# Kernel tuning notes

Measured on AMD Instinct MI355X. Metric: run time of the kernel, lower is better.

Reference implementation:

```python
import jax, jax.numpy as jnp
import numpy as np

DIM = 256          # channels
HEADS = 8
KS = 3             # kernel_size
DIL = (1, 2, 3, 4) # dilation rates
ND = len(DIL)
HEAD_DIM = DIM // HEADS
SCALE = HEAD_DIM ** -0.5
DPG = DIM // ND    # channels per dilation group
EPS = 1e-5


def setup_inputs() -> dict:
    key = jax.random.key(0)
    ks = jax.random.split(key, 4)
    B, H, W = 8, 64, 64
    vi = jax.random.normal(ks[0], (B, DIM, H, W), jnp.float32)
    ir = jax.random.normal(ks[1], (B, DIM, H, W), jnp.float32)
    w_qkv = jax.random.normal(ks[2], (3 * DIM, DIM), jnp.float32) * 0.02  # 1x1 conv, no bias (qkv_bias=False)
    proj_w = jax.random.normal(ks[3], (DIM, DIM), jnp.float32) * 0.02     # nn.Linear weight
    proj_b = jnp.zeros((DIM,), jnp.float32)
    ln_g = jnp.ones((DIM,), jnp.float32)
    ln_b = jnp.zeros((DIM,), jnp.float32)
    return dict(vi=vi, ir=ir, w_qkv=w_qkv, proj_w=proj_w, proj_b=proj_b, ln_g=ln_g, ln_b=ln_b)


def _unfold(t, dil):
    # t: [B, d, H, W] -> [B, d, KS*KS, H, W], same layout as nn.Unfold(KS, dil, pad=dil*(KS-1)//2)
    B, d, H, W = t.shape
    pad = dil * (KS - 1) // 2
    tp = jnp.pad(t, ((0, 0), (0, 0), (pad, pad), (pad, pad)))
    patches = [tp[:, :, i * dil:i * dil + H, j * dil:j * dil + W]
               for i in range(KS) for j in range(KS)]
    return jnp.stack(patches, axis=2)


def _dilate_attention(q, k, v, dil):
    # q,k,v: [B, d, H, W] with d = DPG; returns [B, H, W, d]
    B, d, H, W = q.shape
    h = d // HEAD_DIM
    N = H * W
    kk = KS * KS
    qf = q.reshape(B, h, HEAD_DIM, N)                      # b h d n
    kf = _unfold(k, dil).reshape(B, h, HEAD_DIM, kk, N)    # b h d k n
    vf = _unfold(v, dil).reshape(B, h, HEAD_DIM, kk, N)
    attn = jax.nn.softmax(jnp.einsum('bhdn,bhdkn->bhnk', qf, kf) * SCALE, axis=-1)
    out = jnp.einsum('bhnk,bhdkn->bhnd', attn, vf)         # b h n d
    return out.transpose(0, 2, 1, 3).reshape(B, H, W, d)   # channel = head*HEAD_DIM + c


def _dilate_block(x, w_qkv, proj_w, proj_b, ln_g, ln_b):
    # x: [B, C, H, W]; DilateBlock: permute -> LN -> MultiDilatelocalAttention -> residual -> permute back
    B, C, H, W = x.shape
    xn = x.transpose(0, 2, 3, 1)                           # B H W C
    mu = jnp.mean(xn, -1, keepdims=True)
    var = jnp.var(xn, -1, keepdims=True)
    xn = (xn - mu) * jax.lax.rsqrt(var + EPS) * ln_g + ln_b
    xc = xn.transpose(0, 3, 1, 2)                          # B C H W
    # 1x1 conv qkv -> [B, 3, ND, DPG, H, W]
    qkv = jnp.einsum('oc,bchw->bohw', w_qkv, xc).reshape(B, 3, ND, DPG, H, W)
    outs = [_dilate_attention(qkv[:, 0, i], qkv[:, 1, i], qkv[:, 2, i], DIL[i])
            for i in range(ND)]                            # each [B, H, W, DPG]
    y = jnp.stack(outs, axis=3).reshape(B, H, W, C)        # channel = dil_idx*DPG + c
    y = y @ proj_w.T + proj_b                              # nn.Linear
    return x + y.transpose(0, 3, 1, 2)                     # residual, back to B C H W


def reference(vi, ir, w_qkv, proj_w, proj_b, ln_g, ln_b):
    sub = vi - ir
    div = _dilate_block(sub, w_qkv, proj_w, proj_b, ln_g, ln_b)
    o = jnp.matmul(vi, div)   # batched [H,W]@[H,W] over (B, C)
    return (o, o)
```

## Files before the change

### kernel.cpp

```cpp
#include <hip/hip_runtime.h>
#include <math.h>

#define B_ 8
#define C_ 256
#define N_ 4096
#define NPOS 32768
#define SCALE_ 0.1767766952966369f
#define EPS_ 1e-5f

typedef __attribute__((ext_vector_type(8))) short bf16x8;
typedef __attribute__((ext_vector_type(8))) unsigned short u16x8;
typedef __attribute__((ext_vector_type(4))) float f32x4;

__device__ __forceinline__ unsigned short f2bf(float f) {
  union { float f; unsigned u; } v; v.f = f;
  unsigned r = v.u + 0x7fff + ((v.u >> 16) & 1);
  return (unsigned short)(r >> 16);
}
__device__ __forceinline__ float bf2f(unsigned short u) {
  union { unsigned u; float f; } v; v.u = ((unsigned)u) << 16; return v.f;
}
__device__ __forceinline__ float blo(unsigned u) {
  union { unsigned u; float f; } v; v.u = u << 16; return v.f;
}
__device__ __forceinline__ float bhi(unsigned u) {
  union { unsigned u; float f; } v; v.u = u & 0xffff0000u; return v.f;
}

#define GLD_LDS16(g, l) \
  __builtin_amdgcn_global_load_lds((const __attribute__((address_space(1))) unsigned int*)(g), \
                                   (__attribute__((address_space(3))) unsigned int*)(l), 16, 0, 0)

__global__ __launch_bounds__(256, 4) void k_pre(
    const float* __restrict__ vi, const float* __restrict__ ir,
    const float* __restrict__ wq, const float* __restrict__ pw,
    const float* __restrict__ ln_g, const float* __restrict__ ln_b,
    unsigned short* __restrict__ wdst,
    unsigned short* __restrict__ subB, unsigned short* __restrict__ viB,
    unsigned short* __restrict__ xn)
{
  __shared__ __align__(16) unsigned short tile[32 * 256];
  __shared__ float redS[4][32], redS2[4][32];
  __shared__ float meanS[32], rstdS[32];
  __shared__ float sG[256], sB[256];
  int t = threadIdx.x;
  if (blockIdx.x < 256) {
    int i4 = blockIdx.x * 256 + t;
    float4 v = (i4 < 49152) ? ((const float4*)wq)[i4] : ((const float4*)pw)[i4 - 49152];
    ushort4 o;
    o.x = f2bf(v.x); o.y = f2bf(v.y); o.z = f2bf(v.z); o.w = f2bf(v.w);
    ((ushort4*)wdst)[i4] = o;
    return;
  }
  int blk = blockIdx.x - 256;
  int b = blk >> 7;
  int y = (blk >> 1) & 63;
  int half = blk & 1;
  size_t base = (size_t)b * C_ * N_ + (size_t)y * 64 + half * 32;
  sG[t] = ln_g[t];
  sB[t] = ln_b[t];
  int g = t >> 3;
  int k8 = t & 7;
  int xq = k8 * 4;
  int swz = k8 << 3;

  float4 V[8], I[8];
  #pragma unroll
  for (int it = 0; it < 8; ++it) {
    size_t ga = base + (size_t)(it * 32 + g) * N_ + xq;
    V[it] = *(const float4*)&vi[ga];
  }
  #pragma unroll
  for (int it = 0; it < 8; ++it) {
    size_t ga = base + (size_t)(it * 32 + g) * N_ + xq;
    I[it] = *(const float4*)&ir[ga];
  }

  float s0 = 0.f, s1 = 0.f, s2 = 0.f, s3 = 0.f;
  float q0 = 0.f, q1 = 0.f, q2 = 0.f, q3 = 0.f;
  #pragma unroll
  for (int it = 0; it < 8; ++it) {
    int c = it * 32 + g;
    size_t ga = base + (size_t)c * N_ + xq;
    float4 v4 = V[it];
    float4 i4 = I[it];
    float4 sv;
    sv.x = v4.x - i4.x; sv.y = v4.y - i4.y; sv.z = v4.z - i4.z; sv.w = v4.w - i4.w;
    ushort4 sb, vb;
    sb.x = f2bf(sv.x); sb.y = f2bf(sv.y); sb.z = f2bf(sv.z); sb.w = f2bf(sv.w);
    vb.x = f2bf(v4.x); vb.y = f2bf(v4.y); vb.z = f2bf(v4.z); vb.w = f2bf(v4.w);
    *(ushort4*)&subB[ga] = sb;
    *(ushort4*)&viB[ga] = vb;
    int cs = c ^ swz;
    tile[(xq + 0) * 256 + cs] = sb.x;
    tile[(xq + 1) * 256 + cs] = sb.y;
    tile[(xq + 2) * 256 + cs] = sb.z;
    tile[(xq + 3) * 256 + cs] = sb.w;
    s0 += sv.x; q0 += sv.x * sv.x;
    s1 += sv.y; q1 += sv.y * sv.y;
    s2 += sv.z; q2 += sv.z * sv.z;
    s3 += sv.w; q3 += sv.w * sv.w;
  }
  #pragma unroll
  for (int m = 8; m <= 32; m <<= 1) {
    s0 += __shfl_xor(s0, m); q0 += __shfl_xor(q0, m);
    s1 += __shfl_xor(s1, m); q1 += __shfl_xor(q1, m);
    s2 += __shfl_xor(s2, m); q2 += __shfl_xor(q2, m);
    s3 += __shfl_xor(s3, m); q3 += __shfl_xor(q3, m);
  }
  int w = t >> 6, lt = t & 63;
  if ((lt >> 3) == 0) {
    redS[w][xq + 0] = s0; redS2[w][xq + 0] = q0;
    redS[w][xq + 1] = s1; redS2[w][xq + 1] = q1;
    redS[w][xq + 2] = s2; redS2[w][xq + 2] = q2;
    redS[w][xq + 3] = s3; redS2[w][xq + 3] = q3;
  }
  __syncthreads();
  if (t < 32) {
    float s = redS[0][t] + redS[1][t] + redS[2][t] + redS[3][t];
    float ss = redS2[0][t] + redS2[1][t] + redS2[2][t] + redS2[3][t];
    float mu = s * (1.f / 256.f);
    float var = ss * (1.f / 256.f) - mu * mu;
    meanS[t] = mu;
    rstdS[t] = rsqrtf(var + EPS_);
  }
  __syncthreads();
  int pos = t >> 3;
  float mu = meanS[pos], rs = rstdS[pos];
  int swzr = (pos >> 2) & 7;
  size_t xrow = ((size_t)b * N_ + (size_t)y * 64 + half * 32 + pos) * 256;
  #pragma unroll
  for (int j = 0; j < 4; ++j) {
    int ci = (t & 7) + 8 * j;
    u16x8 tv = *(const u16x8*)&tile[pos * 256 + ((ci ^ swzr) * 8)];
    int c0 = ci * 8;
    u16x8 ov;
    #pragma unroll
    for (int e = 0; e < 8; ++e) {
      float v = bf2f((unsigned short)tv[e]);
      ov[e] = f2bf((v - mu) * rs * sG[c0 + e] + sB[c0 + e]);
    }
    *(u16x8*)&xn[xrow + c0] = ov;
  }
}

template<int EPI, int NT>
__global__ __launch_bounds__(256) void k_gemm_mfma(
    const unsigned short* __restrict__ A,
    const unsigned short* __restrict__ Bw,
    unsigned short* __restrict__ Cout,
    const float* __restrict__ bias,
    const unsigned short* __restrict__ subB,
    int ldc)
{
  __shared__ __align__(16) unsigned short As[128 * 32];
  __shared__ __align__(16) unsigned short Bs[128 * 32];
  __shared__ __align__(16) unsigned short Cs[64 * 136];
  int flat = blockIdx.x;
  int xcd = flat & 7;
  int l = flat >> 3;
  int ml = l / NT;
  int nn = l - ml * NT;
  int m0 = (xcd * 32 + ml) * 128;
  int n0 = nn * 128;
  int tid = threadIdx.x;
  int wv = tid >> 6;
  int lane = tid & 63;
  int mw = (wv >> 1) * 64, nw = (wv & 1) * 64;
  int r = lane & 15, q = lane >> 4;

  int seg0 = wv * 2;
  int srow0 = seg0 * 16 + (lane >> 2);
  int scol = (lane & 3) * 8;
  const unsigned short* ga0 = A  + (size_t)(m0 + srow0) * 256 + scol;
  const unsigned short* ga1 = ga0 + 16 * 256;
  const unsigned short* gb0 = Bw + (size_t)(n0 + srow0) * 256 + scol;
  const unsigned short* gb1 = gb0 + 16 * 256;
  unsigned short* la0 = &As[seg0 * 512];
  unsigned short* la1 = la0 + 512;
  unsigned short* lb0 = &Bs[seg0 * 512];
  unsigned short* lb1 = lb0 + 512;

  f32x4 acc[4][4];
  #pragma unroll
  for (int i = 0; i < 4; ++i)
    #pragma unroll
    for (int j = 0; j < 4; ++j)
      acc[i][j] = (f32x4){0.f, 0.f, 0.f, 0.f};

  for (int k0 = 0; k0 < 256; k0 += 32) {
    GLD_LDS16(ga0 + k0, la0);
    GLD_LDS16(ga1 + k0, la1);
    GLD_LDS16(gb0 + k0, lb0);
    GLD_LDS16(gb1 + k0, lb1);
    __syncthreads();
    bf16x8 af[4], bfr[4];
    #pragma unroll
    for (int mt = 0; mt < 4; ++mt)
      af[mt] = *(const bf16x8*)&As[(mw + mt * 16 + r) * 32 + q * 8];
    #pragma unroll
    for (int nt = 0; nt < 4; ++nt)
      bfr[nt] = *(const bf16x8*)&Bs[(nw + nt * 16 + r) * 32 + q * 8];
    #pragma unroll
    for (int mt = 0; mt < 4; ++mt)
      #pragma unroll
      for (int nt = 0; nt < 4; ++nt)
        acc[mt][nt] = __builtin_amdgcn_mfma_f32_16x16x32_bf16(af[mt], bfr[nt], acc[mt][nt], 0, 0, 0);
    __syncthreads();
  }

  int b = m0 >> 12;
  int nn0 = m0 & 4095;
  #pragma unroll
  for (int pass = 0; pass < 2; ++pass) {
    __syncthreads();
    if (EPI == 0) {
      if ((wv >> 1) == pass) {
        #pragma unroll
        for (int mt = 0; mt < 4; ++mt) {
          int lr = mt * 16 + q * 4;
          #pragma unroll
          for (int nt = 0; nt < 4; ++nt) {
            int col = nw + nt * 16 + r;
            #pragma unroll
            for (int rr = 0; rr < 4; ++rr)
              Cs[(lr + rr) * 136 + col] = f2bf(acc[mt][nt][rr]);
          }
        }
      }
    } else {
      if ((wv & 1) == pass) {
        #pragma unroll
        for (int nt = 0; nt < 4; ++nt) {
          int lr = nt * 16 + r;
          #pragma unroll
          for (int mt = 0; mt < 4; ++mt) {
            int pc = mw + mt * 16 + q * 4;
            #pragma unroll
            for (int rr = 0; rr < 4; ++rr)
              Cs[lr * 136 + pc + rr] = f2bf(acc[mt][nt][rr]);
          }
        }
      }
    }
    __syncthreads();
    if (EPI == 0) {
      #pragma unroll
      for (int cc = 0; cc < 4; ++cc) {
        int ch = cc * 256 + tid;
        int row = ch >> 4, cg = ch & 15;
        u16x8 cv = *(const u16x8*)&Cs[row * 136 + cg * 8];
        int m = m0 + pass * 64 + row;
        *(u16x8*)&Cout[(size_t)m * ldc + n0 + cg * 8] = cv;
      }
    } else {
      #pragma unroll
      for (int cc = 0; cc < 4; ++cc) {
        int ch = cc * 256 + tid;
        int row = ch >> 4, cg = ch & 15;
        u16x8 cv = *(const u16x8*)&Cs[row * 136 + cg * 8];
        int c = n0 + pass * 64 + row;
        size_t idx = ((size_t)(b * 256 + c)) * 4096 + nn0 + cg * 8;
        u16x8 sv = *(const u16x8*)&subB[idx];
        float bb = bias[c];
        u16x8 ov;
        #pragma unroll
        for (int e = 0; e < 8; ++e)
          ov[e] = f2bf(bf2f((unsigned short)cv[e]) + bb + bf2f((unsigned short)sv[e]));
        *(u16x8*)&Cout[idx] = ov;
      }
    }
  }
}

__global__ __launch_bounds__(256) void k_attn(
    const unsigned short* __restrict__ qkv,
    unsigned short* __restrict__ y)
{
  int t = threadIdx.x;
  int sub = t >> 2;
  int lane4 = t & 3;
  int item = blockIdx.x * 64 + sub;
  int ih = item & 7;
  int p = item >> 3;
  int i = ih >> 1, h = ih & 1;
  int dil = i + 1;
  int b = p >> 12;
  int n = p & 4095;
  int py = n >> 6, px = n & 63;
  int off = i * 64 + h * 32 + lane4 * 8;
  const unsigned short* base = qkv + off;

  uint4 qw = *(const uint4*)(base + (size_t)p * 768);
  float q0 = blo(qw.x), q1 = bhi(qw.x), q2 = blo(qw.y), q3 = bhi(qw.y),
        q4 = blo(qw.z), q5 = bhi(qw.z), q6 = blo(qw.w), q7 = bhi(qw.w);

  int pj[9];
  #pragma unroll
  for (int j = 0; j < 9; ++j) {
    int ny = py + (j / 3 - 1) * dil;
    int nx = px + (j % 3 - 1) * dil;
    bool ok = ((unsigned)ny < 64u) && ((unsigned)nx < 64u);
    pj[j] = ok ? ((b << 12) + (ny << 6) + nx) : -1;
  }

  float sc[9];
  #pragma unroll
  for (int j = 0; j < 9; ++j) {
    float s = 0.f;
    if (pj[j] >= 0) {
      uint4 kw = *(const uint4*)(base + 256 + (size_t)pj[j] * 768);
      s  = q0 * blo(kw.x) + q1 * bhi(kw.x);
      s += q2 * blo(kw.y) + q3 * bhi(kw.y);
      s += q4 * blo(kw.z) + q5 * bhi(kw.z);
      s += q6 * blo(kw.w) + q7 * bhi(kw.w);
    }
    s += __shfl_xor(s, 1, 4);
    s += __shfl_xor(s, 2, 4);
    sc[j] = s * SCALE_;
  }

  float mx = sc[0];
  #pragma unroll
  for (int j = 1; j < 9; ++j) mx = fmaxf(mx, sc[j]);
  float e[9], ssum = 0.f;
  #pragma unroll
  for (int j = 0; j < 9; ++j) { e[j] = __expf(sc[j] - mx); ssum += e[j]; }
  float inv = 1.f / ssum;

  float o0 = 0.f, o1 = 0.f, o2 = 0.f, o3 = 0.f, o4 = 0.f, o5 = 0.f, o6 = 0.f, o7 = 0.f;
  #pragma unroll
  for (int j = 0; j < 9; ++j) {
    if (pj[j] >= 0) {
      float w = e[j] * inv;
      uint4 vw = *(const uint4*)(base + 512 + (size_t)pj[j] * 768);
      o0 += w * blo(vw.x); o1 += w * bhi(vw.x);
      o2 += w * blo(vw.y); o3 += w * bhi(vw.y);
      o4 += w * blo(vw.z); o5 += w * bhi(vw.z);
      o6 += w * blo(vw.w); o7 += w * bhi(vw.w);
    }
  }

  u16x8 ov;
  ov[0] = f2bf(o0); ov[1] = f2bf(o1); ov[2] = f2bf(o2); ov[3] = f2bf(o3);
  ov[4] = f2bf(o4); ov[5] = f2bf(o5); ov[6] = f2bf(o6); ov[7] = f2bf(o7);
  *(u16x8*)(y + (size_t)p * 256 + off) = ov;
}

__global__ __launch_bounds__(256) void k_bmm(
    const unsigned short* __restrict__ viB,
    const unsigned short* __restrict__ divmB,
    float* __restrict__ out)
{
  __shared__ __align__(16) unsigned short Vs[64 * 72];
  __shared__ __align__(16) unsigned short Ds[64 * 72];
  int bc = blockIdx.x;
  size_t base = (size_t)bc * 4096;
  int t = threadIdx.x;
  {
    int flat = t * 16;
    int row = flat >> 6, col = flat & 63;
    u16x8 v0 = *(const u16x8*)&viB[base + flat];
    u16x8 v1 = *(const u16x8*)&viB[base + flat + 8];
    *(u16x8*)&Vs[row * 72 + col] = v0;
    *(u16x8*)&Vs[row * 72 + col + 8] = v1;
    u16x8 d0 = *(const u16x8*)&divmB[base + flat];
    u16x8 d1 = *(const u16x8*)&divmB[base + flat + 8];
    #pragma unroll
    for (int e = 0; e < 8; ++e) {
      Ds[(col + e) * 72 + row] = (unsigned short)d0[e];
      Ds[(col + 8 + e) * 72 + row] = (unsigned short)d1[e];
    }
  }
  __syncthreads();
  int w = t >> 6, lane = t & 63;
  int r = lane & 15, q = lane >> 4;
  int wi = (w >> 1) * 32, wj = (w & 1) * 32;
  f32x4 acc[2][2];
  #pragma unroll
  for (int i = 0; i < 2; ++i)
    #pragma unroll
    for (int j = 0; j < 2; ++j)
      acc[i][j] = (f32x4){0.f, 0.f, 0.f, 0.f};
  #pragma unroll
  for (int ks = 0; ks < 2; ++ks) {
    bf16x8 a[2], bfr[2];
    #pragma unroll
    for (int ti = 0; ti < 2; ++ti)
      a[ti] = *(const bf16x8*)&Vs[(wi + ti * 16 + r) * 72 + ks * 32 + q * 8];
    #pragma unroll
    for (int tj = 0; tj < 2; ++tj)
      bfr[tj] = *(const bf16x8*)&Ds[(wj + tj * 16 + r) * 72 + ks * 32 + q * 8];
    #pragma unroll
    for (int ti = 0; ti < 2; ++ti)
      #pragma unroll
      for (int tj = 0; tj < 2; ++tj)
        acc[ti][tj] = __builtin_amdgcn_mfma_f32_16x16x32_bf16(a[ti], bfr[tj], acc[ti][tj], 0, 0, 0);
  }
  #pragma unroll
  for (int ti = 0; ti < 2; ++ti)
    #pragma unroll
    for (int tj = 0; tj < 2; ++tj)
      #pragma unroll
      for (int rr = 0; rr < 4; ++rr) {
        int row = wi + ti * 16 + q * 4 + rr;
        int col = wj + tj * 16 + r;
        float v = acc[ti][tj][rr];
        out[base + row * 64 + col] = v;
        out[8388608ull + base + row * 64 + col] = v;
      }
}

extern "C" void kernel_launch(void* const* d_in, const int* in_sizes, int n_in,
                              void* d_out, int out_size, void* d_ws, size_t ws_size,
                              hipStream_t stream) {
  const float* vi     = (const float*)d_in[0];
  const float* ir     = (const float*)d_in[1];
  const float* w_qkv  = (const float*)d_in[2];
  const float* proj_w = (const float*)d_in[3];
  const float* proj_b = (const float*)d_in[4];
  const float* ln_g   = (const float*)d_in[5];
  const float* ln_b   = (const float*)d_in[6];
  float* out = (float*)d_out;
  char* ws = (char*)d_ws;
  unsigned short* subB = (unsigned short*)(ws);
  unsigned short* qkvb = (unsigned short*)(ws + 16777216);
  unsigned short* divmB= (unsigned short*)(ws + 16777216);
  unsigned short* xnb  = (unsigned short*)(ws + 67108864);
  unsigned short* yb   = (unsigned short*)(ws + 83886080);
  unsigned short* viB  = (unsigned short*)(ws + 100663296);
  unsigned short* wqb  = (unsigned short*)(ws + 117440512);
  unsigned short* pwb  = wqb + 196608;

  k_pre<<<1280, 256, 0, stream>>>(vi, ir, w_qkv, proj_w, ln_g, ln_b, wqb, subB, viB, xnb);
  k_gemm_mfma<0, 6><<<1536, 256, 0, stream>>>(xnb, wqb, qkvb, nullptr, nullptr, 768);
  k_attn<<<4096, 256, 0, stream>>>(qkvb, yb);
  k_gemm_mfma<1, 2><<<512, 256, 0, stream>>>(yb, pwb, divmB, proj_b, subB, 0);
  k_bmm<<<2048, 256, 0, stream>>>(viB, divmB, out);
}
```

Before: 212.1 us.

## Split preprocessing into streaming pass with partial LN stats and separate transpose-normalize kernel

The fused preprocessing kernel is split in two. The first kernel streams vi/ir with fully coalesced 1KB-per-row reads, writes the bf16 sub and vi copies, and stores per-channel-chunk partial sums and sums of squares. A second kernel reduces those partials, reloads the bf16 sub tile, transposes it through LDS and writes the normalized channel-last activations. The aim is better DRAM access patterns for the large fp32 reads, paid for with an extra launch and an extra read of the bf16 sub buffer plus the partials.

Result: no change. 210.9 us (-0.6%).

```diff
diff --git a/kernel.cpp b/kernel.cpp
--- a/kernel.cpp
+++ b/kernel.cpp
@@ -31,116 +31,123 @@
   __builtin_amdgcn_global_load_lds((const __attribute__((address_space(1))) unsigned int*)(g), \
                                    (__attribute__((address_space(3))) unsigned int*)(l), 16, 0, 0)
 
-__global__ __launch_bounds__(256, 4) void k_pre(
+__global__ __launch_bounds__(256, 4) void k_stream(
     const float* __restrict__ vi, const float* __restrict__ ir,
     const float* __restrict__ wq, const float* __restrict__ pw,
-    const float* __restrict__ ln_g, const float* __restrict__ ln_b,
     unsigned short* __restrict__ wdst,
     unsigned short* __restrict__ subB, unsigned short* __restrict__ viB,
-    unsigned short* __restrict__ xn)
+    float2* __restrict__ partials)
 {
-  __shared__ __align__(16) unsigned short tile[32 * 256];
-  __shared__ float redS[4][32], redS2[4][32];
-  __shared__ float meanS[32], rstdS[32];
-  __shared__ float sG[256], sB[256];
   int t = threadIdx.x;
-  if (blockIdx.x < 256) {
-    int i4 = blockIdx.x * 256 + t;
+  int blk = blockIdx.x;
+  if (blk >= 1024) {
+    int i4 = (blk - 1024) * 256 + t;
     float4 v = (i4 < 49152) ? ((const float4*)wq)[i4] : ((const float4*)pw)[i4 - 49152];
     ushort4 o;
     o.x = f2bf(v.x); o.y = f2bf(v.y); o.z = f2bf(v.z); o.w = f2bf(v.w);
     ((ushort4*)wdst)[i4] = o;
     return;
   }
-  int blk = blockIdx.x - 256;
+  __shared__ float redS[4 * 256], redQ[4 * 256];
   int b = blk >> 7;
-  int y = (blk >> 1) & 63;
-  int half = blk & 1;
-  size_t base = (size_t)b * C_ * N_ + (size_t)y * 64 + half * 32;
-  sG[t] = ln_g[t];
-  sB[t] = ln_b[t];
-  int g = t >> 3;
-  int k8 = t & 7;
-  int xq = k8 * 4;
-  int swz = k8 << 3;
+  int chunk = (blk >> 4) & 7;
+  int pgrp = blk & 15;
+  int posq = t & 63;
+  int cg = t >> 6;
+  int c0 = chunk * 32 + cg * 8;
+  int n0 = pgrp * 256 + posq * 4;
+  size_t base = ((size_t)b * C_ + c0) * N_ + n0;
 
   float4 V[8], I[8];
   #pragma unroll
-  for (int it = 0; it < 8; ++it) {
-    size_t ga = base + (size_t)(it * 32 + g) * N_ + xq;
-    V[it] = *(const float4*)&vi[ga];
-  }
-  #pragma unroll
-  for (int it = 0; it < 8; ++it) {
-    size_t ga = base + (size_t)(it * 32 + g) * N_ + xq;
-    I[it] = *(const float4*)&ir[ga];
-  }
+  for (int j = 0; j < 8; ++j) V[j] = *(const float4*)&vi[base + (size_t)j * N_];
+  #pragma unroll
+  for (int j = 0; j < 8; ++j) I[j] = *(const float4*)&ir[base + (size_t)j * N_];
 
   float s0 = 0.f, s1 = 0.f, s2 = 0.f, s3 = 0.f;
   float q0 = 0.f, q1 = 0.f, q2 = 0.f, q3 = 0.f;
   #pragma unroll
-  for (int it = 0; it < 8; ++it) {
-    int c = it * 32 + g;
-    size_t ga = base + (size_t)c * N_ + xq;
-    float4 v4 = V[it];
-    float4 i4 = I[it];
+  for (int j = 0; j < 8; ++j) {
+    float4 v4 = V[j], i4 = I[j];
     float4 sv;
     sv.x = v4.x - i4.x; sv.y = v4.y - i4.y; sv.z = v4.z - i4.z; sv.w = v4.w - i4.w;
     ushort4 sb, vb;
     sb.x = f2bf(sv.x); sb.y = f2bf(sv.y); sb.z = f2bf(sv.z); sb.w = f2bf(sv.w);
     vb.x = f2bf(v4.x); vb.y = f2bf(v4.y); vb.z = f2bf(v4.z); vb.w = f2bf(v4.w);
-    *(ushort4*)&subB[ga] = sb;
-    *(ushort4*)&viB[ga] = vb;
-    int cs = c ^ swz;
-    tile[(xq + 0) * 256 + cs] = sb.x;
-    tile[(xq + 1) * 256 + cs] = sb.y;
-    tile[(xq + 2) * 256 + cs] = sb.z;
-    tile[(xq + 3) * 256 + cs] = sb.w;
+    *(ushort4*)&subB[base + (size_t)j * N_] = sb;
+    *(ushort4*)&viB[base + (size_t)j * N_] = vb;
     s0 += sv.x; q0 += sv.x * sv.x;
     s1 += sv.y; q1 += sv.y * sv.y;
     s2 += sv.z; q2 += sv.z * sv.z;
     s3 += sv.w; q3 += sv.w * sv.w;
   }
-  #pragma unroll
-  for (int m = 8; m <= 32; m <<= 1) {
-    s0 += __shfl_xor(s0, m); q0 += __shfl_xor(q0, m);
-    s1 += __shfl_xor(s1, m); q1 += __shfl_xor(q1, m);
-    s2 += __shfl_xor(s2, m); q2 += __shfl_xor(q2, m);
-    s3 += __shfl_xor(s3, m); q3 += __shfl_xor(q3, m);
-  }
-  int w = t >> 6, lt = t & 63;
-  if ((lt >> 3) == 0) {
-    redS[w][xq + 0] = s0; redS2[w][xq + 0] = q0;
-    redS[w][xq + 1] = s1; redS2[w][xq + 1] = q1;
-    redS[w][xq + 2] = s2; redS2[w][xq + 2] = q2;
-    redS[w][xq + 3] = s3; redS2[w][xq + 3] = q3;
-  }
+  *(f32x4*)&redS[cg * 256 + posq * 4] = (f32x4){s0, s1, s2, s3};
+  *(f32x4*)&redQ[cg * 256 + posq * 4] = (f32x4){q0, q1, q2, q3};
   __syncthreads();
-  if (t < 32) {
-    float s = redS[0][t] + redS[1][t] + redS[2][t] + redS[3][t];
-    float ss = redS2[0][t] + redS2[1][t] + redS2[2][t] + redS2[3][t];
+  float s = redS[t] + redS[256 + t] + redS[512 + t] + redS[768 + t];
+  float q = redQ[t] + redQ[256 + t] + redQ[512 + t] + redQ[768 + t];
+  partials[(size_t)chunk * NPOS + b * 4096 + pgrp * 256 + t] = make_float2(s, q);
+}
+
+__global__ __launch_bounds__(256, 4) void k_lnt(
+    const unsigned short* __restrict__ subB,
+    const float2* __restrict__ partials,
+    const float* __restrict__ ln_g, const float* __restrict__ ln_b,
+    unsigned short* __restrict__ xn)
+{
+  __shared__ __align__(16) unsigned short tile[64 * 256];
+  __shared__ float muS[64], rsS[64];
+  __shared__ float sG[256], sBt[256];
+  int t = threadIdx.x;
+  int blk = blockIdx.x;
+  int b = blk >> 6, pt = blk & 63;
+  int bp0 = b * 4096 + pt * 64;
+  sG[t] = ln_g[t];
+  sBt[t] = ln_b[t];
+  if (t < 64) {
+    float s = 0.f, q = 0.f;
+    #pragma unroll
+    for (int ch = 0; ch < 8; ++ch) {
+      float2 pp = partials[(size_t)ch * NPOS + bp0 + t];
+      s += pp.x; q += pp.y;
+    }
     float mu = s * (1.f / 256.f);
-    float var = ss * (1.f / 256.f) - mu * mu;
-    meanS[t] = mu;
-    rstdS[t] = rsqrtf(var + EPS_);
+    float var = q * (1.f / 256.f) - mu * mu;
+    muS[t] = mu;
+    rsS[t] = rsqrtf(var + EPS_);
+  }
+  int po = t & 7;
+  int c = t >> 3;
+  u16x8 L[8];
+  #pragma unroll
+  for (int it = 0; it < 8; ++it) {
+    int cc = c + it * 32;
+    L[it] = *(const u16x8*)&subB[((size_t)b * C_ + cc) * N_ + pt * 64 + po * 8];
+  }
+  #pragma unroll
+  for (int it = 0; it < 8; ++it) {
+    int cs = (c + it * 32) ^ (po << 3);
+    #pragma unroll
+    for (int e = 0; e < 8; ++e)
+      tile[(po * 8 + e) * 256 + cs] = (unsigned short)L[it][e];
   }
   __syncthreads();
-  int pos = t >> 3;
-  float mu = meanS[pos], rs = rstdS[pos];
-  int swzr = (pos >> 2) & 7;
-  size_t xrow = ((size_t)b * N_ + (size_t)y * 64 + half * 32 + pos) * 256;
-  #pragma unroll
-  for (int j = 0; j < 4; ++j) {
-    int ci = (t & 7) + 8 * j;
-    u16x8 tv = *(const u16x8*)&tile[pos * 256 + ((ci ^ swzr) * 8)];
-    int c0 = ci * 8;
+  int pos8 = t >> 5;
+  int oc = t & 31;
+  #pragma unroll
+  for (int pass = 0; pass < 8; ++pass) {
+    int p = pass * 8 + pos8;
+    float mu = muS[p], rs = rsS[p];
+    int ocs = oc ^ (p >> 3);
+    u16x8 tv = *(const u16x8*)&tile[p * 256 + ocs * 8];
+    int c0 = oc * 8;
     u16x8 ov;
     #pragma unroll
     for (int e = 0; e < 8; ++e) {
       float v = bf2f((unsigned short)tv[e]);
-      ov[e] = f2bf((v - mu) * rs * sG[c0 + e] + sB[c0 + e]);
-    }
-    *(u16x8*)&xn[xrow + c0] = ov;
+      ov[e] = f2bf((v - mu) * rs * sG[c0 + e] + sBt[c0 + e]);
+    }
+    *(u16x8*)&xn[(size_t)(bp0 + p) * 256 + c0] = ov;
   }
 }
 
@@ -425,6 +432,7 @@
   char* ws = (char*)d_ws;
   unsigned short* subB = (unsigned short*)(ws);
   unsigned short* qkvb = (unsigned short*)(ws + 16777216);
+  float2* partials     = (float2*)(ws + 16777216);
   unsigned short* divmB= (unsigned short*)(ws + 16777216);
   unsigned short* xnb  = (unsigned short*)(ws + 67108864);
   unsigned short* yb   = (unsigned short*)(ws + 83886080);
@@ -432,7 +440,8 @@
   unsigned short* wqb  = (unsigned short*)(ws + 117440512);
   unsigned short* pwb  = wqb + 196608;
 
-  k_pre<<<1280, 256, 0, stream>>>(vi, ir, w_qkv, proj_w, ln_g, ln_b, wqb, subB, viB, xnb);
+  k_stream<<<1280, 256, 0, stream>>>(vi, ir, w_qkv, proj_w, wqb, subB, viB, partials);
+  k_lnt<<<512, 256, 0, stream>>>(subB, partials, ln_g, ln_b, xnb);
   k_gemm_mfma<0, 6><<<1536, 256, 0, stream>>>(xnb, wqb, qkvb, nullptr, nullptr, 768);
   k_attn<<<4096, 256, 0, stream>>>(qkvb, yb);
   k_gemm_mfma<1, 2><<<512, 256, 0, stream>>>(yb, pwb, divmB, proj_b, subB, 0);
```
